# Optimization experiments

Measured on AMD Instinct MI355X. Metric: run time of the kernel, lower is better.

## Reference

```python
import jax, jax.numpy as jnp
import numpy as np

N = 128  # image size
J = 4    # number of scales
L = 4    # number of orientations


def make_morlet_filters(n, j_max, n_angles):
    """Fixed Morlet filter bank in Fourier space, shape [J, L, N, N] (real)."""
    freqs = np.fft.fftfreq(n) * 2.0 * np.pi
    kx = freqs[:, None] * np.ones((1, n))
    ky = np.ones((n, 1)) * freqs[None, :]
    filters = np.zeros((j_max, n_angles, n, n), dtype=np.float32)
    for j in range(j_max):
        k0 = 3.0 * np.pi / 4.0 / (2.0 ** j)   # central frequency of scale j
        sigma = 0.8 * (2.0 ** j)               # gaussian width in space
        for l in range(n_angles):
            theta = np.pi * l / n_angles
            k0x, k0y = k0 * np.cos(theta), k0 * np.sin(theta)
            beta = np.exp(-0.5 * sigma ** 2 * k0 ** 2)  # zero-mean correction
            g_shift = np.exp(-0.5 * sigma ** 2 * ((kx - k0x) ** 2 + (ky - k0y) ** 2))
            g_zero = np.exp(-0.5 * sigma ** 2 * (kx ** 2 + ky ** 2))
            filters[j, l] = g_shift - beta * g_zero
    return jnp.asarray(filters)


PSI = make_morlet_filters(N, J, L)  # fixed (non-learned) filter bank
VALID_PAIRS = [(j1, j2) for j1 in range(J) for j2 in range(J) if j2 > j1]  # 6 pairs


def setup_inputs() -> dict:
    key = jax.random.key(0)
    k1, k2, k3, k4, k5 = jax.random.split(key, 5)
    B = 64
    return {
        "image_batch": jax.random.normal(k1, (B, N, N), dtype=jnp.float32),
        "fc1_w": jax.random.normal(k2, (4, 11), dtype=jnp.float32) * 0.3,
        "fc1_b": jax.random.normal(k3, (4,), dtype=jnp.float32) * 0.1,
        "fc2_w": jax.random.normal(k4, (10, 4), dtype=jnp.float32) * 0.3,
        "fc2_b": jax.random.normal(k5, (10,), dtype=jnp.float32) * 0.1,
    }


def _scattering(image):
    # image: [B, N, N]
    i_hat = jnp.fft.fft2(image)  # [B,N,N] complex64
    s0 = jnp.mean(image, axis=(1, 2))  # [B]
    # first order: |x * psi_{j1,l1}|  -> [B,J,L,N,N]
    u1 = jnp.abs(jnp.fft.ifft2(i_hat[:, None, None] * PSI[None]))
    s1 = jnp.mean(u1, axis=(2, 3, 4))  # [B,J] averaged over orientations+space
    u1_hat = jnp.fft.fft2(u1)  # [B,J,L,N,N]
    # second order: only j2 > j1 (others NaN in original and masked out)
    s2_list = []
    for (j1, j2) in VALID_PAIRS:
        # [B, L1, L2, N, N]
        field = jnp.fft.ifft2(u1_hat[:, j1, :, None] * PSI[j2][None, None])
        s2_list.append(jnp.mean(jnp.abs(field), axis=(1, 2, 3, 4)))
    s2 = jnp.stack(s2_list, axis=1)  # [B,6]
    return jnp.concatenate([s0[:, None], s1, s2], axis=1)  # [B,11]


def reference(image_batch, fc1_w, fc1_b, fc2_w, fc2_b):
    coeffs = _scattering(image_batch)                      # [B,11]
    h = jax.nn.relu(coeffs @ fc1_w.T + fc1_b)              # [B,4]
    return jax.nn.sigmoid(h @ fc2_w.T + fc2_b)             # [B,10]
```

## Files before the change

### kernel.cpp

```cpp
#include <hip/hip_runtime.h>
#include <math.h>

#define NN   128
#define SS   129
#define TT   512
#define NPIX 16384
#define EPT  32
#define SG   65
#define SG32 33


__device__ __forceinline__ float2 cmul(float2 a, float2 w) {
    return make_float2(a.x * w.x - a.y * w.y, a.x * w.y + a.y * w.x);
}
__device__ __forceinline__ float2 cmulc(float2 a, float2 w) {
    return make_float2(a.x * w.x + a.y * w.y, a.y * w.x - a.x * w.y);
}

template<int SGN>
__device__ __forceinline__ void fft4(float2* f) {
    float2 t0 = make_float2(f[0].x + f[2].x, f[0].y + f[2].y);
    float2 t1 = make_float2(f[0].x - f[2].x, f[0].y - f[2].y);
    float2 t2 = make_float2(f[1].x + f[3].x, f[1].y + f[3].y);
    float2 t3 = make_float2(f[1].x - f[3].x, f[1].y - f[3].y);
// ... 380 lines not shown
        int fb = blk - 256;
        int f = fb >> 3, chunk = fb & 7;
        int j = f >> 2, l = f & 3;
        float k0    = 2.35619449019234493f / (float)(1 << j);
        float sigma = 0.8f * (float)(1 << j);
        float s2    = sigma * sigma;
        float theta = 0.78539816339744831f * (float)l;
        float k0x = k0 * cosf(theta);
        float k0y = k0 * sinf(theta);
        float beta = expf(-0.5f * s2 * k0 * k0);
        const float FSTEP = 0.04908738521234052f;
        float* dst = psi + (size_t)f * NPIX;
        int i0 = chunk * 2048, i1 = i0 + 2048;
        for (int i = i0 + tid; i < i1; i += TT) {
            int pr = i >> 7, pc = i & 127;
            int kr = (pr >> 4) + 8 * (pr & 15);
            int kc = (pc >> 4) + 8 * (pc & 15);
            float fr = (float)(kr < 64 ? kr : kr - 128) * FSTEP;
            float fc = (float)(kc < 64 ? kc : kc - 128) * FSTEP;
            float dx = fr - k0x, dy = fc - k0y;
            float g1 = expf(-0.5f * s2 * (dx * dx + dy * dy));
            float g0 = expf(-0.5f * s2 * (fr * fr + fc * fc));
            dst[i] = g1 - beta * g0;
        }
        return;
    }
    int b = blk >> 2, q = blk & 3;
    buildTw(tw, tid);
    const float* im = img + (size_t)b * NPIX + (size_t)q * 32 * NN;
    #pragma unroll
    for (int k = 0; k < 8; ++k) {
        int e = k * TT + tid;
        F[(e >> 7) * SS + (e & 127)] = make_float2(im[e], 0.f);
    }
    __syncthreads();
    {
        int x = tid & 31, t = tid >> 5;
        float2* M = F + x * SS;
        float2 f[8];
        #pragma unroll
        for (int n1 = 0; n1 < 8; ++n1) f[n1] = M[t + 16 * n1];
        fft8<-1>(f);
        #pragma unroll
        for (int ka = 0; ka < 8; ++ka)
            M[t + 16 * ka] = cmulc(f[ka], tw[t * ka]);
    }
    __syncthreads();
    if (tid < 256) {
        int x = tid & 31, ka = tid >> 5;
        float2* M = F + x * SS + 16 * ka;
        float2 g[16];
        #pragma unroll
        for (int t = 0; t < 16; ++t) g[t] = M[t];
        fft16<-1>(g);
        #pragma unroll
        for (int kb = 0; kb < 16; ++kb) M[kb] = g[kb];
    }
    __syncthreads();
    float2* dst = interm + (size_t)b * NPIX + (size_t)q * 32 * NN;
    #pragma unroll
    for (int k = 0; k < 8; ++k) {
        int e = k * TT + tid;
        dst[e] = F[(e >> 7) * SS + (e & 127)];
    }
}

__global__ __attribute__((amdgpu_flat_work_group_size(TT, TT), amdgpu_waves_per_eu(4, 4)))
void k_pre2(float2* __restrict__ ihat,
            float* __restrict__ coeffs) {
    __shared__ __align__(16) float2 F[128 * 33];
    __shared__ float2 tw[128];
    int blk = blockIdx.x, tid = threadIdx.x;
    int b = blk >> 2, q = blk & 3;
    buildTw(tw, tid);
    float2* base = ihat + (size_t)b * NPIX + q * 32;
    #pragma unroll
    for (int k = 0; k < 8; ++k) {
        int e = k * TT + tid;
        int r = e >> 5, cl = e & 31;
        F[r * 33 + cl] = base[r * NN + cl];
    }
    __syncthreads();
    {
        int cl = tid & 31, t = tid >> 5;
        float2 f[8];
        #pragma unroll
        for (int n1 = 0; n1 < 8; ++n1) f[n1] = F[(t + 16 * n1) * 33 + cl];
        fft8<-1>(f);
        #pragma unroll
        for (int ka = 0; ka < 8; ++ka)
            F[(t + 16 * ka) * 33 + cl] = cmulc(f[ka], tw[t * ka]);
    }
    __syncthreads();
    if (tid < 256) {
        int cl = tid & 31, ka = tid >> 5;
        float2 g[16];
        #pragma unroll
        for (int t = 0; t < 16; ++t) g[t] = F[(16 * ka + t) * 33 + cl];
        fft16<-1>(g);
        float2* dst = base + cl;
        #pragma unroll
        for (int kb = 0; kb < 16; ++kb)
            dst[(16 * ka + kb) * NN] = g[kb];
        if (q == 0 && cl == 0 && ka == 0)
            coeffs[b * 11 + 0] = g[0].x * (1.f / 16384.f);
    }
}

__global__ __attribute__((amdgpu_flat_work_group_size(TT, TT), amdgpu_waves_per_eu(2, 2)))
void k_scat_big(const float2* __restrict__ ihat,
                const float* __restrict__ psi,
                float* __restrict__ coeffs,
                float2* __restrict__ Hg) {
    __shared__ __align__(16) float2 F[16640];
    __shared__ float2 tw[128];
    float2* G2a = F;
    float2* G2b = F + 4160;
    float2* G2c = F + 8320;
    float2* G2d = F + 12480;
    int tid = threadIdx.x;
    int x = blockIdx.x;
    int b = x & 63, l1 = x >> 6;
    const float2* ih = ihat + (size_t)b * NPIX;
    const float*  p1 = psi + (size_t)l1 * NPIX;
    buildTw(tw, tid);

    const float S1_128 = 9.3132257461547852e-10f;
    const float S2TR   = 5.6843418860808015e-14f;

    int kalo = tid >> 7, c = tid & 127;
    {
        #pragma unroll
        for (int i = 0; i < 2; ++i) {
            int ka = kalo + 4 * i;
            float2 g[16];
            #pragma unroll
            for (int kb = 0; kb < 16; ++kb) {
                int e = (16 * ka + kb) * NN + c;
                float2 z = ih[e];
                float  p = p1[e];
                g[kb] = make_float2(z.x * p, z.y * p);
            }
            fft16<1>(g);
            #pragma unroll
            for (int t = 0; t < 16; ++t)
                F[(16 * ka + t) * SS + c] = cmul(g[t], tw[t * ka]);
        }
    }
    __syncthreads();
    invB<SS, 1>(F, tid);      __syncthreads();
    invA<1, SS>(F, tw, tid);  __syncthreads();
    float acc = 0.f;
    invBmag_fwdA_row(F, tw, tid, acc);
    float ws1 = waveReduceSum(acc);
    if ((tid & 63) == 0) atomicAdd(&coeffs[b * 11 + 1], ws1 * S1_128);
    __syncthreads();
    fwdB<1, SS>(F, tid);      __syncthreads();
    fwdA<SS, 1>(F, tw, tid);  __syncthreads();
    float2 uh[32];
    fwdB_col_capture(F, tid, uh);
    __syncthreads();

    int m = c & 15;
    bool colKeep = (m < 4) || (m >= 12);
    int pc64 = 8 * (c >> 4) + ((m < 4) ? m : (m - 8));
    int fc = (c >> 4) + 8 * (c & 15);

    {
        float2* Hf = Hg + ((size_t)(b * 4 + l1)) * 4096;
        if (colKeep) {
            #pragma unroll
            for (int i = 0; i < 2; ++i) {
                int ka = kalo + 4 * i;
                #pragma unroll
                for (int kb = 0; kb < 16; ++kb) {
                    if (kb < 4 || kb >= 12) {
                        int pr64 = 8 * ka + ((kb < 4) ? kb : (kb - 8));
                        Hf[pr64 * 64 + pc64] = uh[i * 16 + kb];
                    }
                }
            }
        }
    }

    {
        const int ORW[4] = {21, 15, 0, -15};
        const int OCW[4] = { 0, 15, 21,  15};
        bool ckw[4]; int pcw[4];
        #pragma unroll
        for (int w = 0; w < 4; ++w) {
            int dc = (fc - OCW[w]) & 127;
            ckw[w] = (dc < 32) || (dc >= 96);
            int uc = (dc < 32) ? dc : (dc - 64);
            pcw[w] = 8 * (uc & 7) + (uc >> 3);
        }
        #pragma unroll
        for (int i = 0; i < 2; ++i) {
            int ka = kalo + 4 * i;
            #pragma unroll
            for (int kb = 0; kb < 16; ++kb) {
                int fr = ka + 8 * kb;
                float2 z = uh[i * 16 + kb];
                int e = (16 * ka + kb) * NN + c;
                #pragma unroll
                for (int w = 0; w < 4; ++w) {
                    if (ckw[w]) {
                        int dr = (fr - ORW[w]) & 127;
                        if (dr < 32 || dr >= 96) {
                            int ur = (dr < 32) ? dr : (dr - 64);
                            int pr = 8 * (ur & 7) + (ur >> 3);
                            float pv = psi[(size_t)(4 + w) * NPIX + e];
                            float2* G = (w == 0) ? G2a : (w == 1) ? G2b
                                       : (w == 2) ? G2c : G2d;
                            G[pr * SG + pcw[w]] = make_float2(z.x * pv, z.y * pv);
                        }
                    }
                }
            }
        }
        __syncthreads();
        {
            int col = tid & 63, k8 = tid >> 6;
            float2 f0[8], f1[8], f2[8], f3[8];
            #pragma unroll
            for (int kb = 0; kb < 8; ++kb) {
                int o = (8 * k8 + kb) * SG + col;
                f0[kb] = G2a[o]; f1[kb] = G2b[o]; f2[kb] = G2c[o]; f3[kb] = G2d[o];
            }
            fft8<1>(f0); fft8<1>(f1); fft8<1>(f2); fft8<1>(f3);
            #pragma unroll
            for (int q = 0; q < 8; ++q) {
                float2 w = tw[2 * q * k8];
                int o = (8 * k8 + q) * SG + col;
                G2a[o] = cmul(f0[q], w); G2b[o] = cmul(f1[q], w);
                G2c[o] = cmul(f2[q], w); G2d[o] = cmul(f3[q], w);
            }
        }
        __syncthreads();
        {
            int col = tid & 63, q = tid >> 6;
            float2 f0[8], f1[8], f2[8], f3[8];
            #pragma unroll
            for (int k8 = 0; k8 < 8; ++k8) {
                int o = (8 * k8 + q) * SG + col;
                f0[k8] = G2a[o]; f1[k8] = G2b[o]; f2[k8] = G2c[o]; f3[k8] = G2d[o];
            }
            fft8<1>(f0); fft8<1>(f1); fft8<1>(f2); fft8<1>(f3);
            #pragma unroll
            for (int n1 = 0; n1 < 8; ++n1) {
                int o = (8 * n1 + q) * SG + col;
                G2a[o] = f0[n1]; G2b[o] = f1[n1]; G2c[o] = f2[n1]; G2d[o] = f3[n1];
            }
        }
        __syncthreads();
        {
            int row = tid & 63, k8 = tid >> 6;
            int base = row * SG + 8 * k8;
            float2 f0[8], f1[8], f2[8], f3[8];
            #pragma unroll
            for (int kb = 0; kb < 8; ++kb) {
                f0[kb] = G2a[base + kb]; f1[kb] = G2b[base + kb];
                f2[kb] = G2c[base + kb]; f3[kb] = G2d[base + kb];
            }
            fft8<1>(f0); fft8<1>(f1); fft8<1>(f2); fft8<1>(f3);
            #pragma unroll
            for (int q = 0; q < 8; ++q) {
                float2 w = tw[2 * q * k8];
                G2a[base + q] = cmul(f0[q], w); G2b[base + q] = cmul(f1[q], w);
                G2c[base + q] = cmul(f2[q], w); G2d[base + q] = cmul(f3[q], w);
            }
        }
        __syncthreads();
        float a2 = 0.f;
        {
            int row = tid & 63, q = tid >> 6;
            int base = row * SG + q;
            float2 f0[8], f1[8], f2[8], f3[8];
            #pragma unroll
            for (int k8 = 0; k8 < 8; ++k8) {
                int o = base + 8 * k8;
                f0[k8] = G2a[o]; f1[k8] = G2b[o]; f2[k8] = G2c[o]; f3[k8] = G2d[o];
            }
            fft8<1>(f0); fft8<1>(f1); fft8<1>(f2); fft8<1>(f3);
            #pragma unroll
            for (int n1 = 0; n1 < 8; ++n1) {
                a2 += sqrtf(f0[n1].x * f0[n1].x + f0[n1].y * f0[n1].y);
                a2 += sqrtf(f1[n1].x * f1[n1].x + f1[n1].y * f1[n1].y);
                a2 += sqrtf(f2[n1].x * f2[n1].x + f2[n1].y * f2[n1].y);
                a2 += sqrtf(f3[n1].x * f3[n1].x + f3[n1].y * f3[n1].y);
            }
        }
        float ws2 = waveReduceSum(a2);
        if ((tid & 63) == 0) atomicAdd(&coeffs[b * 11 + 5 + 0], ws2 * S2TR);
    }
}

__global__ __attribute__((amdgpu_flat_work_group_size(TT, TT), amdgpu_waves_per_eu(4, 4)))
void k_scat_small(const float2* __restrict__ ihat,
                  const float* __restrict__ psi,
                  float* __restrict__ coeffs,
                  const float2* __restrict__ Hg) {
    __shared__ __align__(16) float2 S[8448];
    __shared__ float2 tw[128];
    float2* G2  = S;
    float2* G32 = S;
    float2* Qs0 = S;
    float2* Qs1 = S + 1056;
    float2* Qs2 = S + 2112;
    float2* Qs3 = S + 3168;
    float4* Psa = (float4*)(S + 4224);
    float4* Psb = (float4*)(S + 6336);
    int tid = threadIdx.x;
    int x = blockIdx.x;
    int b = x & 63, l1 = (x >> 6) & 3;
    int t0 = x >> 8;
    const float2* ih = ihat + (size_t)b * NPIX;
    const float*  p1 = psi + (size_t)(((t0 == 0) ? 1 : ((t0 == 2) ? 2 : 3)) * 4 + l1) * NPIX;
    buildTw(tw, tid);

    const float S1_64 = 3.7252902984619141e-9f;
    const float S1_32 = 1.4901161193847656e-8f;
    const float S2_32 = 9.0949470177292824e-13f;

    int kalo = tid >> 7, c = tid & 127;

    if (t0 == 1) {
        const float S2_03 = 2.2737367544323206e-13f;
        const float2* Hf = Hg + ((size_t)(b * 4 + l1)) * 4096;
        int m = c & 15;
        bool colKeep = (m < 4) || (m >= 12);
        int pc64 = 8 * (c >> 4) + ((m < 4) ? m : (m - 8));
        int fc = (c >> 4) + 8 * (c & 15);
        const int OR2[4] = {9, 6, 0, -6};
        const int OC2[4] = {0, 6, 9,  6};
        bool ckq[4]; int pcq[4];
        #pragma unroll
        for (int w = 0; w < 4; ++w) {
            int dc = (fc - OC2[w]) & 127;
            ckq[w] = (dc < 16) || (dc >= 112);
            int f32c = (dc < 16) ? dc : (dc - 96);
            pcq[w] = 4 * (f32c & 7) + (f32c >> 3);
        }
        bool ck32 = (m < 2) || (m >= 14);
        int pc32 = 4 * (c >> 4) + ((m < 2) ? m : (m - 12));
        const float* p20 = psi + (size_t)8 * NPIX;
        const float* p30 = psi + (size_t)12 * NPIX;
        if (colKeep) {
            #pragma unroll
            for (int i = 0; i < 2; ++i) {
                int ka = kalo + 4 * i;
                #pragma unroll
                for (int kb = 0; kb < 16; ++kb) {
                    if (kb < 4 || kb >= 12) {
                        int pr64 = 8 * ka + ((kb < 4) ? kb : (kb - 8));
                        float2 z = Hf[pr64 * 64 + pc64];
                        int fr = ka + 8 * kb;
                        int e = (16 * ka + kb) * NN + c;
                        #pragma unroll
                        for (int w = 0; w < 4; ++w) {
                            if (ckq[w]) {
                                int dr = (fr - OR2[w]) & 127;
                                if (dr < 16 || dr >= 112) {
                                    int f32r = (dr < 16) ? dr : (dr - 96);
                                    int pr = 4 * (f32r & 7) + (f32r >> 3);
                                    float pv = p20[(size_t)w * NPIX + e];
                                    float2* Q = (w == 0) ? Qs0 : (w == 1) ? Qs1
                                               : (w == 2) ? Qs2 : Qs3;
                                    Q[pr * SG32 + pcq[w]] = make_float2(z.x * pv, z.y * pv);
                                }
                            }
                        }
                        if (ck32 && (kb < 2 || kb >= 14)) {
                            int pr32 = 4 * ka + ((kb < 2) ? kb : (kb - 12));
                            float a0 = p30[e], a1 = p30[NPIX + e];
                            float a2f = p30[2 * NPIX + e], a3 = p30[3 * NPIX + e];
                            Psa[pr32 * SG32 + pc32] =
                                make_float4(z.x * a0, z.y * a0, z.x * a1, z.y * a1);
                            Psb[pr32 * SG32 + pc32] =
                                make_float4(z.x * a2f, z.y * a2f, z.x * a3, z.y * a3);
                        }
                    }
                }
            }
        }
        float aq, ap;
        pass32combo(Qs0, Qs1, Qs2, Qs3, Psa, Psb, tw, tid, aq, ap);
        float wsq = waveReduceSum(aq);
        float wsp = waveReduceSum(ap);
        if ((tid & 63) == 0) {
            atomicAdd(&coeffs[b * 11 + 5 + 1], wsq * S2_03);
            atomicAdd(&coeffs[b * 11 + 5 + 2], wsp * S2_03);
        }
        return;
    }

    if (t0 == 0) {
        const int OR1[4] = {21, 15, 0, -15};
        const int OC1[4] = { 0, 15, 21,  15};
        int fc = (c >> 4) + 8 * (c & 15);
        int dc = (fc - OC1[l1]) & 127;
        bool ck = (dc < 32) || (dc >= 96);
        int ucw = (dc < 32) ? dc : (dc - 64);
        int pcd = 8 * (ucw & 7) + (ucw >> 3);
        if (ck) {
            #pragma unroll
            for (int i = 0; i < 2; ++i) {
                int ka = kalo + 4 * i;
                #pragma unroll
                for (int kb = 0; kb < 16; ++kb) {
                    int fr = ka + 8 * kb;
                    int dr = (fr - OR1[l1]) & 127;
                    if (dr < 32 || dr >= 96) {
                        int ur = (dr < 32) ? dr : (dr - 64);
                        int pr = 8 * (ur & 7) + (ur >> 3);
                        int e = (16 * ka + kb) * NN + c;
                        float2 z = ih[e];
                        float  p = p1[e];
                        G2[pr * SG + pcd] = make_float2(z.x * p, z.y * p);
                    }
                }
            }
        }
        __syncthreads();
        {
            int col = tid & 63, k8 = tid >> 6;
            float2 f[8];
            #pragma unroll
            for (int kb = 0; kb < 8; ++kb) f[kb] = G2[(8 * k8 + kb) * SG + col];
            fft8<1>(f);
            #pragma unroll
            for (int q = 0; q < 8; ++q)
                G2[(8 * k8 + q) * SG + col] = cmul(f[q], tw[2 * q * k8]);
        }
        __syncthreads();
        {
            int col = tid & 63, q = tid >> 6;
            float2 f[8];
            #pragma unroll
            for (int k8 = 0; k8 < 8; ++k8) f[k8] = G2[(8 * k8 + q) * SG + col];
            fft8<1>(f);
            #pragma unroll
            for (int n1 = 0; n1 < 8; ++n1) G2[(8 * n1 + q) * SG + col] = f[n1];
        }
        __syncthreads();
        {
            int row = tid & 63, k8 = tid >> 6;
            float2* R = G2 + row * SG + 8 * k8;
            float2 f[8];
            #pragma unroll
            for (int kb = 0; kb < 8; ++kb) f[kb] = R[kb];
            fft8<1>(f);
            #pragma unroll
            for (int q = 0; q < 8; ++q) R[q] = cmul(f[q], tw[2 * q * k8]);
        }
        __syncthreads();
        float acc = 0.f;
        {
            int row = tid & 63, q = tid >> 6;
            float2* R = G2 + row * SG + q;
            float2 f[8];
            #pragma unroll
            for (int k8 = 0; k8 < 8; ++k8) f[k8] = R[8 * k8];
            fft8<1>(f);
            #pragma unroll
            for (int n1 = 0; n1 < 8; ++n1) {
                float mg = sqrtf(f[n1].x * f[n1].x + f[n1].y * f[n1].y);
                acc += mg;
                f[n1] = make_float2(mg, 0.f);
            }
            fft8<-1>(f);
            #pragma unroll
            for (int ka = 0; ka < 8; ++ka)
                R[8 * ka] = cmulc(f[ka], tw[2 * q * ka]);
        }
        float ws1 = waveReduceSum(acc);
        if ((tid & 63) == 0) atomicAdd(&coeffs[b * 11 + 2], ws1 * S1_64);
        __syncthreads();
        {
            int row2 = tid & 63, ka = tid >> 6;
            float2* R2 = G2 + row2 * SG + 8 * ka;
            float2 g[8];
            #pragma unroll
            for (int t = 0; t < 8; ++t) g[t] = R2[t];
            fft8<-1>(g);
            #pragma unroll
            for (int kb = 0; kb < 8; ++kb) R2[kb] = g[kb];
        }
        __syncthreads();
        {
            int col = tid & 63, t = tid >> 6;
            float2 g[8];
            #pragma unroll
            for (int n1 = 0; n1 < 8; ++n1) g[n1] = G2[(t + 8 * n1) * SG + col];
            fft8<-1>(g);
            #pragma unroll
            for (int ka = 0; ka < 8; ++ka)
                G2[(t + 8 * ka) * SG + col] = cmulc(g[ka], tw[2 * t * ka]);
        }
        __syncthreads();
        float2 vh[8];
        int c6 = tid & 63, ka8 = tid >> 6;
        {
            float2 g[8];
            #pragma unroll
            for (int t = 0; t < 8; ++t) g[t] = G2[(8 * ka8 + t) * SG + c6];
            fft8<-1>(g);
            #pragma unroll
            for (int kb = 0; kb < 8; ++kb) vh[kb] = g[kb];
        }
        __syncthreads();

        int uc64 = 8 * (c6 & 7) + (c6 >> 3);
        int fc128 = (uc64 < 32) ? uc64 : (uc64 + 64);
        int scI = 16 * (fc128 & 7) + (fc128 >> 3);
        int se[8];
        #pragma unroll
        for (int kb = 0; kb < 8; ++kb) {
            int ur = 8 * kb + ka8;
            int fr128 = (ur < 32) ? ur : (ur + 64);
            se[kb] = (16 * (fr128 & 7) + (fr128 >> 3)) * NN + scI;
        }

        {
            const int OR2[4] = {9, 6, 0, -6};
            const int OC2[4] = {0, 6, 9,  6};
            bool ckq[4]; int pcq[4];
            #pragma unroll
            for (int w = 0; w < 4; ++w) {
                int dcw = (uc64 - OC2[w]) & 63;
                ckq[w] = (dcw < 16) || (dcw >= 48);
                int f32c = (dcw < 16) ? dcw : (dcw - 32);
                pcq[w] = 4 * (f32c & 7) + (f32c >> 3);
            }
            int m6 = c6 & 7;
            bool ckV = (m6 < 2) || (m6 >= 6);
            int p32c = 4 * (c6 >> 3) + ((m6 < 2) ? m6 : (m6 - 4));
            const float* p30 = psi + (size_t)12 * NPIX;
            #pragma unroll
            for (int kb = 0; kb < 8; ++kb) {
                int ur = 8 * kb + ka8;
                float2 z = vh[kb];
                int e = se[kb];
                #pragma unroll
                for (int w = 0; w < 4; ++w) {
                    if (ckq[w]) {
                        int dr = (ur - OR2[w]) & 63;
                        if (dr < 16 || dr >= 48) {
                            int f32r = (dr < 16) ? dr : (dr - 32);
                            int pr = 4 * (f32r & 7) + (f32r >> 3);
                            float pv = psi[(size_t)(8 + w) * NPIX + e];
                            float2* Q = (w == 0) ? Qs0 : (w == 1) ? Qs1
                                       : (w == 2) ? Qs2 : Qs3;
                            Q[pr * SG32 + pcq[w]] = make_float2(z.x * pv, z.y * pv);
                        }
                    }
                }
                if (ckV && (kb < 2 || kb >= 6)) {
                    int pr32 = 4 * ka8 + (kb & 3);
                    float a0 = p30[e], a1 = p30[NPIX + e];
                    float a2f = p30[2 * NPIX + e], a3 = p30[3 * NPIX + e];
                    Psa[pr32 * SG32 + p32c] =
                        make_float4(z.x * a0, z.y * a0, z.x * a1, z.y * a1);
                    Psb[pr32 * SG32 + p32c] =
                        make_float4(z.x * a2f, z.y * a2f, z.x * a3, z.y * a3);
                }
            }
            float aq, ap;
            pass32combo(Qs0, Qs1, Qs2, Qs3, Psa, Psb, tw, tid, aq, ap);
            float wsq = waveReduceSum(aq);
            float wsp = waveReduceSum(ap);
            if ((tid & 63) == 0) {
                atomicAdd(&coeffs[b * 11 + 5 + 3], wsq * S2_32);
                atomicAdd(&coeffs[b * 11 + 5 + 4], wsp * S2_32);
            }
        }
        return;
    }

    if (t0 == 3) {
        int m = c & 15;
        bool ck32 = (m < 2) || (m >= 14);
        int pc32 = 4 * (c >> 4) + ((m < 2) ? m : (m - 12));
        if (ck32) {
            #pragma unroll
            for (int i = 0; i < 2; ++i) {
                int ka = kalo + 4 * i;
                #pragma unroll
                for (int kb = 0; kb < 16; ++kb) {
                    if (kb < 2 || kb >= 14) {
                        int e = (16 * ka + kb) * NN + c;
                        float2 z = ih[e];
                        float  p = p1[e];
                        int pr32 = 4 * ka + ((kb < 2) ? kb : (kb - 12));
                        G32[pr32 * SG32 + pc32] = make_float2(z.x * p, z.y * p);
                    }
                }
            }
        }
        __syncthreads();
        if (tid < 256) {
            int line = tid & 31, a = tid >> 5;
            float2 f[4];
            #pragma unroll
            for (int kb = 0; kb < 4; ++kb) f[kb] = G32[(4 * a + kb) * SG32 + line];
            fft4<1>(f);
            #pragma unroll
            for (int t = 0; t < 4; ++t)
                G32[(4 * a + t) * SG32 + line] = cmul(f[t], tw[4 * t * a]);
        }
        __syncthreads();
        if (tid < 128) {
            int line = tid & 31, t = tid >> 5;
            float2 f[8];
            #pragma unroll
            for (int a = 0; a < 8; ++a) f[a] = G32[(4 * a + t) * SG32 + line];
            fft8<1>(f);
            #pragma unroll
            for (int n1 = 0; n1 < 8; ++n1) G32[(4 * n1 + t) * SG32 + line] = f[n1];
        }
        __syncthreads();
        if (tid < 256) {
            int row = tid & 31, a = tid >> 5;
            float2* R = G32 + row * SG32 + 4 * a;
            float2 f[4];
            #pragma unroll
            for (int kb = 0; kb < 4; ++kb) f[kb] = R[kb];
            fft4<1>(f);
            #pragma unroll
            for (int t = 0; t < 4; ++t) R[t] = cmul(f[t], tw[4 * t * a]);
        }
        __syncthreads();
        float acc = 0.f;
        if (tid < 128) {
            int row = tid & 31, t = tid >> 5;
            float2* R = G32 + row * SG32 + t;
            float2 f[8];
            #pragma unroll
            for (int a = 0; a < 8; ++a) f[a] = R[4 * a];
            fft8<1>(f);
            #pragma unroll
            for (int n1 = 0; n1 < 8; ++n1)
                acc += sqrtf(f[n1].x * f[n1].x + f[n1].y * f[n1].y);
        }
        float ws1 = waveReduceSum(acc);
        if ((tid & 63) == 0 && tid < 128) atomicAdd(&coeffs[b * 11 + 4], ws1 * S1_32);
        return;
    }

    {
        const float S2_23 = 3.6379788070917130e-12f;
        const int OR1[4] = {9, 6, 0, -6};
        const int OC1[4] = {0, 6, 9,  6};
        float2* G = S;
        float4* Pa = (float4*)(S + 1088);
        float4* Pb = (float4*)(S + 3200);
        int fc = (c >> 4) + 8 * (c & 15);
        int dc = (fc - OC1[l1]) & 127;
        bool ck = (dc < 16) || (dc >= 112);
        int f32c = (dc < 16) ? dc : (dc - 96);
        int pcd = 4 * (f32c & 7) + (f32c >> 3);
        if (ck) {
            #pragma unroll
            for (int i = 0; i < 2; ++i) {
                int ka = kalo + 4 * i;
                #pragma unroll
                for (int kb = 0; kb < 16; ++kb) {
                    int fr = ka + 8 * kb;
                    int dr = (fr - OR1[l1]) & 127;
                    if (dr < 16 || dr >= 112) {
                        int f32r = (dr < 16) ? dr : (dr - 96);
                        int pr = 4 * (f32r & 7) + (f32r >> 3);
                        int e = (16 * ka + kb) * NN + c;
                        float2 z = ih[e];
                        float  p = p1[e];
                        G[pr * SG32 + pcd] = make_float2(z.x * p, z.y * p);
                    }
                }
            }
        }
        __syncthreads();
        if (tid < 256) {
            int line = tid & 31, a = tid >> 5;
            float2 f[4];
            #pragma unroll
            for (int kb = 0; kb < 4; ++kb) f[kb] = G[(4 * a + kb) * SG32 + line];
            fft4<1>(f);
            #pragma unroll
            for (int t = 0; t < 4; ++t)
                G[(4 * a + t) * SG32 + line] = cmul(f[t], tw[4 * t * a]);
        }
        __syncthreads();
        if (tid < 128) {
            int line = tid & 31, t = tid >> 5;
            float2 f[8];
            #pragma unroll
            for (int a = 0; a < 8; ++a) f[a] = G[(4 * a + t) * SG32 + line];
            fft8<1>(f);
            #pragma unroll
            for (int n1 = 0; n1 < 8; ++n1) G[(4 * n1 + t) * SG32 + line] = f[n1];
        }
        __syncthreads();
        if (tid < 256) {
            int row = tid & 31, a = tid >> 5;
            float2* R = G + row * SG32 + 4 * a;
            float2 f[4];
            #pragma unroll
            for (int kb = 0; kb < 4; ++kb) f[kb] = R[kb];
            fft4<1>(f);
            #pragma unroll
            for (int t = 0; t < 4; ++t) R[t] = cmul(f[t], tw[4 * t * a]);
        }
        __syncthreads();
        float acc = 0.f;
        if (tid < 128) {
            int row = tid & 31, t = tid >> 5;
            float2* R = G + row * SG32 + t;
            float2 f[8];
            #pragma unroll
            for (int a = 0; a < 8; ++a) f[a] = R[4 * a];
            fft8<1>(f);
            #pragma unroll
            for (int n1 = 0; n1 < 8; ++n1) {
                float mg = sqrtf(f[n1].x * f[n1].x + f[n1].y * f[n1].y);
                acc += mg;
                R[4 * n1] = make_float2(mg, 0.f);
            }
        }
        float ws1 = waveReduceSum(acc);
        if ((tid & 63) == 0 && tid < 128) atomicAdd(&coeffs[b * 11 + 3], ws1 * S1_32);
        __syncthreads();
        if (tid < 256) {
            int row = tid & 31, a = tid >> 5;
            float2* R = G + row * SG32 + 4 * a;
            float2 f[4];
            #pragma unroll
            for (int kb = 0; kb < 4; ++kb) f[kb] = R[kb];
            fft4<-1>(f);
            #pragma unroll
            for (int t = 0; t < 4; ++t) R[t] = cmulc(f[t], tw[4 * t * a]);
        }
        __syncthreads();
        if (tid < 128) {
            int row = tid & 31, t = tid >> 5;
            float2* R = G + row * SG32 + t;
            float2 f[8];
            #pragma unroll
            for (int a = 0; a < 8; ++a) f[a] = R[4 * a];
            fft8<-1>(f);
            #pragma unroll
            for (int n1 = 0; n1 < 8; ++n1) R[4 * n1] = f[n1];
        }
        __syncthreads();
        if (tid < 256) {
            int line = tid & 31, a = tid >> 5;
            float2 f[4];
            #pragma unroll
            for (int kb = 0; kb < 4; ++kb) f[kb] = G[(4 * a + kb) * SG32 + line];
            fft4<-1>(f);
            #pragma unroll
            for (int t = 0; t < 4; ++t)
                G[(4 * a + t) * SG32 + line] = cmulc(f[t], tw[4 * t * a]);
        }
        __syncthreads();
        if (tid < 128) {
            int line = tid & 31, t = tid >> 5;
            float2 f[8];
            #pragma unroll
            for (int a = 0; a < 8; ++a) f[a] = G[(4 * a + t) * SG32 + line];
            fft8<-1>(f);
            #pragma unroll
            for (int n1 = 0; n1 < 8; ++n1) G[(4 * n1 + t) * SG32 + line] = f[n1];
        }
        __syncthreads();
        {
            const float* q0 = psi + (size_t)12 * NPIX;
            const float* q1 = q0 + NPIX;
            const float* q2 = q1 + NPIX;
            const float* q3 = q2 + NPIX;
            #pragma unroll
            for (int ii = 0; ii < 2; ++ii) {
                int s = ii * 512 + tid;
                int pr = s >> 5, pc = s & 31;
                int ur = (pr >> 2) + 8 * (pr & 3);
                int uc = (pc >> 2) + 8 * (pc & 3);
                int fr = (ur < 16) ? ur : (ur + 96);
                int fcc = (uc < 16) ? uc : (uc + 96);
                int e = (16 * (fr & 7) + (fr >> 3)) * NN
                      + 16 * (fcc & 7) + (fcc >> 3);
                float2 z = G[pr * SG32 + pc];
                float a0 = q0[e], a1 = q1[e], a2f = q2[e], a3 = q3[e];
                Pa[pr * SG32 + pc] = make_float4(z.x * a0, z.y * a0, z.x * a1, z.y * a1);
                Pb[pr * SG32 + pc] = make_float4(z.x * a2f, z.y * a2f, z.x * a3, z.y * a3);
            }
        }
        float a2 = pass32x4(Pa, Pb, tw, tid);
        float ws2 = waveReduceSum(a2);
        if ((tid & 63) == 0) atomicAdd(&coeffs[b * 11 + 5 + 5], ws2 * S2_23);
    }
}

__global__ void k_mlp(const float* __restrict__ coeffs,
                      const float* __restrict__ w1, const float* __restrict__ b1,
                      const float* __restrict__ w2, const float* __restrict__ b2,
                      float* __restrict__ out) {
    int b = threadIdx.x;
    if (b >= 64) return;
    float c[11];
    #pragma unroll
    for (int i = 0; i < 11; ++i) c[i] = coeffs[b * 11 + i];
    float h[4];
    #pragma unroll
    for (int k = 0; k < 4; ++k) {
        float s = b1[k];
        #pragma unroll
        for (int i = 0; i < 11; ++i) s += w1[k * 11 + i] * c[i];
        h[k] = fmaxf(s, 0.f);
    }
    #pragma unroll
    for (int o = 0; o < 10; ++o) {
        float s = b2[o];
        #pragma unroll
        for (int k = 0; k < 4; ++k) s += w2[o * 4 + k] * h[k];
        out[b * 10 + o] = 1.f / (1.f + expf(-s));
    }
}

extern "C" void kernel_launch(void* const* d_in, const int* in_sizes, int n_in,
                              void* d_out, int out_size, void* d_ws, size_t ws_size,
                              hipStream_t stream) {
    const float* img = (const float*)d_in[0];
    const float* w1  = (const float*)d_in[1];
    const float* b1  = (const float*)d_in[2];
    const float* w2  = (const float*)d_in[3];
    const float* b2  = (const float*)d_in[4];
    float* out = (float*)d_out;

    float*  ws     = (float*)d_ws;
    float*  psi    = ws;
    float2* ihat   = (float2*)(ws + 16 * NPIX);
    float2* Hg     = ihat + (size_t)64 * NPIX;
    float*  coeffs = ws + 16 * NPIX + 2 * 64 * NPIX + 2 * 256 * 4096;

    hipLaunchKernelGGL(k_pre1,       dim3(385),  dim3(TT), 0, stream, img, psi, ihat, coeffs);
    hipLaunchKernelGGL(k_pre2,       dim3(256),  dim3(TT), 0, stream, ihat, coeffs);
    hipLaunchKernelGGL(k_scat_big,   dim3(256),  dim3(TT), 0, stream, ihat, psi, coeffs, Hg);
    hipLaunchKernelGGL(k_scat_small, dim3(1024), dim3(TT), 0, stream, ihat, psi, coeffs, Hg);
    hipLaunchKernelGGL(k_mlp,        dim3(1),    dim3(64), 0, stream, coeffs, w1, b1, w2, b2, out);
}
```

Baseline: 167.9 us.

## Pair j1=1 orientations per block and schedule heavy blocks first

The j1=1 scattering branch now has each block process two orientations. The two orientations share the image-spectrum loads, and the block runs both 64x64 FFT pipelines in lockstep between the same barriers. The second-order stage then loops over the two fields, reusing the shared-memory scratch. Block indices are remapped so these heavier blocks come first in the grid, which shrinks from 1024 to 896 blocks. The aim is to cut redundant global loads and reduce tail imbalance, at the cost of longer per-block critical paths and higher register pressure.

```diff
diff --git a/kernel.cpp b/kernel.cpp
--- a/kernel.cpp
+++ b/kernel.cpp
@@ -706,7 +706,6 @@
                   const float2* __restrict__ Hg) {
     __shared__ __align__(16) float2 S[8448];
     __shared__ float2 tw[128];
-    float2* G2  = S;
     float2* G32 = S;
     float2* Qs0 = S;
     float2* Qs1 = S + 1056;
@@ -716,10 +715,6 @@
     float4* Psb = (float4*)(S + 6336);
     int tid = threadIdx.x;
     int x = blockIdx.x;
-    int b = x & 63, l1 = (x >> 6) & 3;
-    int t0 = x >> 8;
-    const float2* ih = ihat + (size_t)b * NPIX;
-    const float*  p1 = psi + (size_t)(((t0 == 0) ? 1 : ((t0 == 2) ? 2 : 3)) * 4 + l1) * NPIX;
     buildTw(tw, tid);
 
     const float S1_64 = 3.7252902984619141e-9f;
@@ -728,7 +723,298 @@
 
     int kalo = tid >> 7, c = tid & 127;
 
-    if (t0 == 1) {
+    if (x < 128) {
+        int b = x & 63, ph = x >> 6;
+        int l1a = 2 * ph, l1b = 2 * ph + 1;
+        const float2* ih = ihat + (size_t)b * NPIX;
+        const float* p1a = psi + (size_t)(4 + l1a) * NPIX;
+        const float* p1b = psi + (size_t)(4 + l1b) * NPIX;
+        float2* G2A = S;
+        float2* G2B = S + 4160;
+        const int OR1[4] = {21, 15, 0, -15};
+        const int OC1[4] = { 0, 15, 21,  15};
+        int fc = (c >> 4) + 8 * (c & 15);
+        int dcA = (fc - OC1[l1a]) & 127;
+        bool ckA = (dcA < 32) || (dcA >= 96);
+        int ucwA = (dcA < 32) ? dcA : (dcA - 64);
+        int pcdA = 8 * (ucwA & 7) + (ucwA >> 3);
+        int dcB = (fc - OC1[l1b]) & 127;
+        bool ckB = (dcB < 32) || (dcB >= 96);
+        int ucwB = (dcB < 32) ? dcB : (dcB - 64);
+        int pcdB = 8 * (ucwB & 7) + (ucwB >> 3);
+        #pragma unroll
+        for (int i = 0; i < 2; ++i) {
+            int ka = kalo + 4 * i;
+            #pragma unroll
+            for (int kb = 0; kb < 16; ++kb) {
+                int fr = ka + 8 * kb;
+                int e = (16 * ka + kb) * NN + c;
+                float2 z = ih[e];
+                if (ckA) {
+                    int dr = (fr - OR1[l1a]) & 127;
+                    if (dr < 32 || dr >= 96) {
+                        int ur = (dr < 32) ? dr : (dr - 64);
+                        int pr = 8 * (ur & 7) + (ur >> 3);
+                        float p = p1a[e];
+                        G2A[pr * SG + pcdA] = make_float2(z.x * p, z.y * p);
+                    }
+                }
+                if (ckB) {
+                    int dr = (fr - OR1[l1b]) & 127;
+                    if (dr < 32 || dr >= 96) {
+                        int ur = (dr < 32) ? dr : (dr - 64);
+                        int pr = 8 * (ur & 7) + (ur >> 3);
+                        float p = p1b[e];
+                        G2B[pr * SG + pcdB] = make_float2(z.x * p, z.y * p);
+                    }
+                }
+            }
+        }
+        __syncthreads();
+        {
+            int col = tid & 63, k8 = tid >> 6;
+            {
+                float2 f[8];
+                #pragma unroll
+                for (int kb = 0; kb < 8; ++kb) f[kb] = G2A[(8 * k8 + kb) * SG + col];
+                fft8<1>(f);
+                #pragma unroll
+                for (int q = 0; q < 8; ++q)
+                    G2A[(8 * k8 + q) * SG + col] = cmul(f[q], tw[2 * q * k8]);
+            }
+            {
+                float2 f[8];
+                #pragma unroll
+                for (int kb = 0; kb < 8; ++kb) f[kb] = G2B[(8 * k8 + kb) * SG + col];
+                fft8<1>(f);
+                #pragma unroll
+                for (int q = 0; q < 8; ++q)
+                    G2B[(8 * k8 + q) * SG + col] = cmul(f[q], tw[2 * q * k8]);
+            }
+        }
+        __syncthreads();
+        {
+            int col = tid & 63, q = tid >> 6;
+            {
+                float2 f[8];
+                #pragma unroll
+                for (int k8 = 0; k8 < 8; ++k8) f[k8] = G2A[(8 * k8 + q) * SG + col];
+                fft8<1>(f);
+                #pragma unroll
+                for (int n1 = 0; n1 < 8; ++n1) G2A[(8 * n1 + q) * SG + col] = f[n1];
+            }
+            {
+                float2 f[8];
+                #pragma unroll
+                for (int k8 = 0; k8 < 8; ++k8) f[k8] = G2B[(8 * k8 + q) * SG + col];
+                fft8<1>(f);
+                #pragma unroll
+                for (int n1 = 0; n1 < 8; ++n1) G2B[(8 * n1 + q) * SG + col] = f[n1];
+            }
+        }
+        __syncthreads();
+        {
+            int row = tid & 63, k8 = tid >> 6;
+            {
+                float2* R = G2A + row * SG + 8 * k8;
+                float2 f[8];
+                #pragma unroll
+                for (int kb = 0; kb < 8; ++kb) f[kb] = R[kb];
+                fft8<1>(f);
+                #pragma unroll
+                for (int q = 0; q < 8; ++q) R[q] = cmul(f[q], tw[2 * q * k8]);
+            }
+            {
+                float2* R = G2B + row * SG + 8 * k8;
+                float2 f[8];
+                #pragma unroll
+                for (int kb = 0; kb < 8; ++kb) f[kb] = R[kb];
+                fft8<1>(f);
+                #pragma unroll
+                for (int q = 0; q < 8; ++q) R[q] = cmul(f[q], tw[2 * q * k8]);
+            }
+        }
+        __syncthreads();
+        float acc = 0.f;
+        {
+            int row = tid & 63, q = tid >> 6;
+            {
+                float2* R = G2A + row * SG + q;
+                float2 f[8];
+                #pragma unroll
+                for (int k8 = 0; k8 < 8; ++k8) f[k8] = R[8 * k8];
+                fft8<1>(f);
+                #pragma unroll
+                for (int n1 = 0; n1 < 8; ++n1) {
+                    float mg = sqrtf(f[n1].x * f[n1].x + f[n1].y * f[n1].y);
+                    acc += mg;
+                    f[n1] = make_float2(mg, 0.f);
+                }
+                fft8<-1>(f);
+                #pragma unroll
+                for (int ka = 0; ka < 8; ++ka)
+                    R[8 * ka] = cmulc(f[ka], tw[2 * q * ka]);
+            }
+            {
+                float2* R = G2B + row * SG + q;
+                float2 f[8];
+                #pragma unroll
+                for (int k8 = 0; k8 < 8; ++k8) f[k8] = R[8 * k8];
+                fft8<1>(f);
+                #pragma unroll
+                for (int n1 = 0; n1 < 8; ++n1) {
+                    float mg = sqrtf(f[n1].x * f[n1].x + f[n1].y * f[n1].y);
+                    acc += mg;
+                    f[n1] = make_float2(mg, 0.f);
+                }
+                fft8<-1>(f);
+                #pragma unroll
+                for (int ka = 0; ka < 8; ++ka)
+                    R[8 * ka] = cmulc(f[ka], tw[2 * q * ka]);
+            }
+        }
+        float ws1 = waveReduceSum(acc);
+        if ((tid & 63) == 0) atomicAdd(&coeffs[b * 11 + 2], ws1 * S1_64);
+        __syncthreads();
+        {
+            int row2 = tid & 63, ka = tid >> 6;
+            {
+                float2* R2 = G2A + row2 * SG + 8 * ka;
+                float2 g[8];
+                #pragma unroll
+                for (int t = 0; t < 8; ++t) g[t] = R2[t];
+                fft8<-1>(g);
+                #pragma unroll
+                for (int kb = 0; kb < 8; ++kb) R2[kb] = g[kb];
+            }
+            {
+                float2* R2 = G2B + row2 * SG + 8 * ka;
+                float2 g[8];
+                #pragma unroll
+                for (int t = 0; t < 8; ++t) g[t] = R2[t];
+                fft8<-1>(g);
+                #pragma unroll
+                for (int kb = 0; kb < 8; ++kb) R2[kb] = g[kb];
+            }
+        }
+        __syncthreads();
+        {
+            int col = tid & 63, t = tid >> 6;
+            {
+                float2 g[8];
+                #pragma unroll
+                for (int n1 = 0; n1 < 8; ++n1) g[n1] = G2A[(t + 8 * n1) * SG + col];
+                fft8<-1>(g);
+                #pragma unroll
+                for (int ka = 0; ka < 8; ++ka)
+                    G2A[(t + 8 * ka) * SG + col] = cmulc(g[ka], tw[2 * t * ka]);
+            }
+            {
+                float2 g[8];
+                #pragma unroll
+                for (int n1 = 0; n1 < 8; ++n1) g[n1] = G2B[(t + 8 * n1) * SG + col];
+                fft8<-1>(g);
+                #pragma unroll
+                for (int ka = 0; ka < 8; ++ka)
+                    G2B[(t + 8 * ka) * SG + col] = cmulc(g[ka], tw[2 * t * ka]);
+            }
+        }
+        __syncthreads();
+        float2 vhA[8], vhB[8];
+        int c6 = tid & 63, ka8 = tid >> 6;
+        {
+            {
+                float2 g[8];
+                #pragma unroll
+                for (int t = 0; t < 8; ++t) g[t] = G2A[(8 * ka8 + t) * SG + c6];
+                fft8<-1>(g);
+                #pragma unroll
+                for (int kb = 0; kb < 8; ++kb) vhA[kb] = g[kb];
+            }
+            {
+                float2 g[8];
+                #pragma unroll
+                for (int t = 0; t < 8; ++t) g[t] = G2B[(8 * ka8 + t) * SG + c6];
+                fft8<-1>(g);
+                #pragma unroll
+                for (int kb = 0; kb < 8; ++kb) vhB[kb] = g[kb];
+            }
+        }
+        __syncthreads();
+
+        int uc64 = 8 * (c6 & 7) + (c6 >> 3);
+        int fc128 = (uc64 < 32) ? uc64 : (uc64 + 64);
+        int scI = 16 * (fc128 & 7) + (fc128 >> 3);
+        int se[8];
+        #pragma unroll
+        for (int kb = 0; kb < 8; ++kb) {
+            int ur = 8 * kb + ka8;
+            int fr128 = (ur < 32) ? ur : (ur + 64);
+            se[kb] = (16 * (fr128 & 7) + (fr128 >> 3)) * NN + scI;
+        }
+        const int OR2[4] = {9, 6, 0, -6};
+        const int OC2[4] = {0, 6, 9,  6};
+        bool ckq[4]; int pcq[4];
+        #pragma unroll
+        for (int w = 0; w < 4; ++w) {
+            int dcw = (uc64 - OC2[w]) & 63;
+            ckq[w] = (dcw < 16) || (dcw >= 48);
+            int f32c = (dcw < 16) ? dcw : (dcw - 32);
+            pcq[w] = 4 * (f32c & 7) + (f32c >> 3);
+        }
+        int m6 = c6 & 7;
+        bool ckV = (m6 < 2) || (m6 >= 6);
+        int p32c = 4 * (c6 >> 3) + ((m6 < 2) ? m6 : (m6 - 4));
+        const float* p30 = psi + (size_t)12 * NPIX;
+
+        #pragma unroll
+        for (int fld = 0; fld < 2; ++fld) {
+            const float2* vh = (fld == 0) ? vhA : vhB;
+            #pragma unroll
+            for (int kb = 0; kb < 8; ++kb) {
+                int ur = 8 * kb + ka8;
+                float2 z = vh[kb];
+                int e = se[kb];
+                #pragma unroll
+                for (int w = 0; w < 4; ++w) {
+                    if (ckq[w]) {
+                        int dr = (ur - OR2[w]) & 63;
+                        if (dr < 16 || dr >= 48) {
+                            int f32r = (dr < 16) ? dr : (dr - 32);
+                            int pr = 4 * (f32r & 7) + (f32r >> 3);
+                            float pv = psi[(size_t)(8 + w) * NPIX + e];
+                            float2* Q = (w == 0) ? Qs0 : (w == 1) ? Qs1
+                                       : (w == 2) ? Qs2 : Qs3;
+                            Q[pr * SG32 + pcq[w]] = make_float2(z.x * pv, z.y * pv);
+                        }
+                    }
+                }
+                if (ckV && (kb < 2 || kb >= 6)) {
+                    int pr32 = 4 * ka8 + (kb & 3);
+                    float a0 = p30[e], a1 = p30[NPIX + e];
+                    float a2f = p30[2 * NPIX + e], a3 = p30[3 * NPIX + e];
+                    Psa[pr32 * SG32 + p32c] =
+                        make_float4(z.x * a0, z.y * a0, z.x * a1, z.y * a1);
+                    Psb[pr32 * SG32 + p32c] =
+                        make_float4(z.x * a2f, z.y * a2f, z.x * a3, z.y * a3);
+                }
+            }
+            float aq, ap;
+            pass32combo(Qs0, Qs1, Qs2, Qs3, Psa, Psb, tw, tid, aq, ap);
+            float wsq = waveReduceSum(aq);
+            float wsp = waveReduceSum(ap);
+            if ((tid & 63) == 0) {
+                atomicAdd(&coeffs[b * 11 + 5 + 3], wsq * S2_32);
+                atomicAdd(&coeffs[b * 11 + 5 + 4], wsp * S2_32);
+            }
+            __syncthreads();
+        }
+        return;
+    }
+
+    if (x < 384) {
+        int y = x - 128;
+        int b = y & 63, l1 = y >> 6;
         const float S2_03 = 2.2737367544323206e-13f;
         const float2* Hf = Hg + ((size_t)(b * 4 + l1)) * 4096;
         int m = c & 15;
@@ -798,260 +1084,11 @@
         return;
     }
 
-    if (t0 == 0) {
-        const int OR1[4] = {21, 15, 0, -15};
-        const int OC1[4] = { 0, 15, 21,  15};
-        int fc = (c >> 4) + 8 * (c & 15);
-        int dc = (fc - OC1[l1]) & 127;
-        bool ck = (dc < 32) || (dc >= 96);
-        int ucw = (dc < 32) ? dc : (dc - 64);
-        int pcd = 8 * (ucw & 7) + (ucw >> 3);
-        if (ck) {
-            #pragma unroll
-            for (int i = 0; i < 2; ++i) {
-                int ka = kalo + 4 * i;
-                #pragma unroll
-                for (int kb = 0; kb < 16; ++kb) {
-                    int fr = ka + 8 * kb;
-                    int dr = (fr - OR1[l1]) & 127;
-                    if (dr < 32 || dr >= 96) {
-                        int ur = (dr < 32) ? dr : (dr - 64);
-                        int pr = 8 * (ur & 7) + (ur >> 3);
-                        int e = (16 * ka + kb) * NN + c;
-                        float2 z = ih[e];
-                        float  p = p1[e];
-                        G2[pr * SG + pcd] = make_float2(z.x * p, z.y * p);
-                    }
-                }
-            }
-        }
-        __syncthreads();
-        {
-            int col = tid & 63, k8 = tid >> 6;
-            float2 f[8];
-            #pragma unroll
-            for (int kb = 0; kb < 8; ++kb) f[kb] = G2[(8 * k8 + kb) * SG + col];
-            fft8<1>(f);
-            #pragma unroll
-            for (int q = 0; q < 8; ++q)
-                G2[(8 * k8 + q) * SG + col] = cmul(f[q], tw[2 * q * k8]);
-        }
-        __syncthreads();
-        {
-            int col = tid & 63, q = tid >> 6;
-            float2 f[8];
-            #pragma unroll
-            for (int k8 = 0; k8 < 8; ++k8) f[k8] = G2[(8 * k8 + q) * SG + col];
-            fft8<1>(f);
-            #pragma unroll
-            for (int n1 = 0; n1 < 8; ++n1) G2[(8 * n1 + q) * SG + col] = f[n1];
-        }
-        __syncthreads();
-        {
-            int row = tid & 63, k8 = tid >> 6;
-            float2* R = G2 + row * SG + 8 * k8;
-            float2 f[8];
-            #pragma unroll
-            for (int kb = 0; kb < 8; ++kb) f[kb] = R[kb];
-            fft8<1>(f);
-            #pragma unroll
-            for (int q = 0; q < 8; ++q) R[q] = cmul(f[q], tw[2 * q * k8]);
-        }
-        __syncthreads();
-        float acc = 0.f;
-        {
-            int row = tid & 63, q = tid >> 6;
-            float2* R = G2 + row * SG + q;
-            float2 f[8];
-            #pragma unroll
-            for (int k8 = 0; k8 < 8; ++k8) f[k8] = R[8 * k8];
-            fft8<1>(f);
-            #pragma unroll
-            for (int n1 = 0; n1 < 8; ++n1) {
-                float mg = sqrtf(f[n1].x * f[n1].x + f[n1].y * f[n1].y);
-                acc += mg;
-                f[n1] = make_float2(mg, 0.f);
-            }
-            fft8<-1>(f);
-            #pragma unroll
-            for (int ka = 0; ka < 8; ++ka)
-                R[8 * ka] = cmulc(f[ka], tw[2 * q * ka]);
-        }
-        float ws1 = waveReduceSum(acc);
-        if ((tid & 63) == 0) atomicAdd(&coeffs[b * 11 + 2], ws1 * S1_64);
-        __syncthreads();
-        {
-            int row2 = tid & 63, ka = tid >> 6;
-            float2* R2 = G2 + row2 * SG + 8 * ka;
-            float2 g[8];
-            #pragma unroll
-            for (int t = 0; t < 8; ++t) g[t] = R2[t];
-            fft8<-1>(g);
-            #pragma unroll
-            for (int kb = 0; kb < 8; ++kb) R2[kb] = g[kb];
-        }
-        __syncthreads();
-        {
-            int col = tid & 63, t = tid >> 6;
-            float2 g[8];
-            #pragma unroll
-            for (int n1 = 0; n1 < 8; ++n1) g[n1] = G2[(t + 8 * n1) * SG + col];
-            fft8<-1>(g);
-            #pragma unroll
-            for (int ka = 0; ka < 8; ++ka)
-                G2[(t + 8 * ka) * SG + col] = cmulc(g[ka], tw[2 * t * ka]);
-        }
-        __syncthreads();
-        float2 vh[8];
-        int c6 = tid & 63, ka8 = tid >> 6;
-        {
-            float2 g[8];
-            #pragma unroll
-            for (int t = 0; t < 8; ++t) g[t] = G2[(8 * ka8 + t) * SG + c6];
-            fft8<-1>(g);
-            #pragma unroll
-            for (int kb = 0; kb < 8; ++kb) vh[kb] = g[kb];
-        }
-        __syncthreads();
-
-        int uc64 = 8 * (c6 & 7) + (c6 >> 3);
-        int fc128 = (uc64 < 32) ? uc64 : (uc64 + 64);
-        int scI = 16 * (fc128 & 7) + (fc128 >> 3);
-        int se[8];
-        #pragma unroll
-        for (int kb = 0; kb < 8; ++kb) {
-            int ur = 8 * kb + ka8;
-            int fr128 = (ur < 32) ? ur : (ur + 64);
-            se[kb] = (16 * (fr128 & 7) + (fr128 >> 3)) * NN + scI;
-        }
-
-        {
-            const int OR2[4] = {9, 6, 0, -6};
-            const int OC2[4] = {0, 6, 9,  6};
-            bool ckq[4]; int pcq[4];
-            #pragma unroll
-            for (int w = 0; w < 4; ++w) {
-                int dcw = (uc64 - OC2[w]) & 63;
-                ckq[w] = (dcw < 16) || (dcw >= 48);
-                int f32c = (dcw < 16) ? dcw : (dcw - 32);
-                pcq[w] = 4 * (f32c & 7) + (f32c >> 3);
-            }
-            int m6 = c6 & 7;
-            bool ckV = (m6 < 2) || (m6 >= 6);
-            int p32c = 4 * (c6 >> 3) + ((m6 < 2) ? m6 : (m6 - 4));
-            const float* p30 = psi + (size_t)12 * NPIX;
-            #pragma unroll
-            for (int kb = 0; kb < 8; ++kb) {
-                int ur = 8 * kb + ka8;
-                float2 z = vh[kb];
-                int e = se[kb];
-                #pragma unroll
-                for (int w = 0; w < 4; ++w) {
-                    if (ckq[w]) {
-                        int dr = (ur - OR2[w]) & 63;
-                        if (dr < 16 || dr >= 48) {
-                            int f32r = (dr < 16) ? dr : (dr - 32);
-                            int pr = 4 * (f32r & 7) + (f32r >> 3);
-                            float pv = psi[(size_t)(8 + w) * NPIX + e];
-                            float2* Q = (w == 0) ? Qs0 : (w == 1) ? Qs1
-                                       : (w == 2) ? Qs2 : Qs3;
-                            Q[pr * SG32 + pcq[w]] = make_float2(z.x * pv, z.y * pv);
-                        }
-                    }
-                }
-                if (ckV && (kb < 2 || kb >= 6)) {
-                    int pr32 = 4 * ka8 + (kb & 3);
-                    float a0 = p30[e], a1 = p30[NPIX + e];
-                    float a2f = p30[2 * NPIX + e], a3 = p30[3 * NPIX + e];
-                    Psa[pr32 * SG32 + p32c] =
-                        make_float4(z.x * a0, z.y * a0, z.x * a1, z.y * a1);
-                    Psb[pr32 * SG32 + p32c] =
-                        make_float4(z.x * a2f, z.y * a2f, z.x * a3, z.y * a3);
-                }
-            }
-            float aq, ap;
-            pass32combo(Qs0, Qs1, Qs2, Qs3, Psa, Psb, tw, tid, aq, ap);
-            float wsq = waveReduceSum(aq);
-            float wsp = waveReduceSum(ap);
-            if ((tid & 63) == 0) {
-                atomicAdd(&coeffs[b * 11 + 5 + 3], wsq * S2_32);
-                atomicAdd(&coeffs[b * 11 + 5 + 4], wsp * S2_32);
-            }
-        }
-        return;
-    }
-
-    if (t0 == 3) {
-        int m = c & 15;
-        bool ck32 = (m < 2) || (m >= 14);
-        int pc32 = 4 * (c >> 4) + ((m < 2) ? m : (m - 12));
-        if (ck32) {
-            #pragma unroll
-            for (int i = 0; i < 2; ++i) {
-                int ka = kalo + 4 * i;
-                #pragma unroll
-                for (int kb = 0; kb < 16; ++kb) {
-                    if (kb < 2 || kb >= 14) {
-                        int e = (16 * ka + kb) * NN + c;
-                        float2 z = ih[e];
-                        float  p = p1[e];
-                        int pr32 = 4 * ka + ((kb < 2) ? kb : (kb - 12));
-                        G32[pr32 * SG32 + pc32] = make_float2(z.x * p, z.y * p);
-                    }
-                }
-            }
-        }
-        __syncthreads();
-        if (tid < 256) {
-            int line = tid & 31, a = tid >> 5;
-            float2 f[4];
-            #pragma unroll
-            for (int kb = 0; kb < 4; ++kb) f[kb] = G32[(4 * a + kb) * SG32 + line];
-            fft4<1>(f);
-            #pragma unroll
-            for (int t = 0; t < 4; ++t)
-                G32[(4 * a + t) * SG32 + line] = cmul(f[t], tw[4 * t * a]);
-        }
-        __syncthreads();
-        if (tid < 128) {
-            int line = tid & 31, t = tid >> 5;
-            float2 f[8];
-            #pragma unroll
-            for (int a = 0; a < 8; ++a) f[a] = G32[(4 * a + t) * SG32 + line];
-            fft8<1>(f);
-            #pragma unroll
-            for (int n1 = 0; n1 < 8; ++n1) G32[(4 * n1 + t) * SG32 + line] = f[n1];
-        }
-        __syncthreads();
-        if (tid < 256) {
-            int row = tid & 31, a = tid >> 5;
-            float2* R = G32 + row * SG32 + 4 * a;
-            float2 f[4];
-            #pragma unroll
-            for (int kb = 0; kb < 4; ++kb) f[kb] = R[kb];
-            fft4<1>(f);
-            #pragma unroll
-            for (int t = 0; t < 4; ++t) R[t] = cmul(f[t], tw[4 * t * a]);
-        }
-        __syncthreads();
-        float acc = 0.f;
-        if (tid < 128) {
-            int row = tid & 31, t = tid >> 5;
-            float2* R = G32 + row * SG32 + t;
-            float2 f[8];
-            #pragma unroll
-            for (int a = 0; a < 8; ++a) f[a] = R[4 * a];
-            fft8<1>(f);
-            #pragma unroll
-            for (int n1 = 0; n1 < 8; ++n1)
-                acc += sqrtf(f[n1].x * f[n1].x + f[n1].y * f[n1].y);
-        }
-        float ws1 = waveReduceSum(acc);
-        if ((tid & 63) == 0 && tid < 128) atomicAdd(&coeffs[b * 11 + 4], ws1 * S1_32);
-        return;
-    }
-
-    {
+    if (x < 640) {
+        int y = x - 384;
+        int b = y & 63, l1 = y >> 6;
+        const float2* ih = ihat + (size_t)b * NPIX;
+        const float* p1 = psi + (size_t)(8 + l1) * NPIX;
         const float S2_23 = 3.6379788070917130e-12f;
         const int OR1[4] = {9, 6, 0, -6};
         const int OC1[4] = {0, 6, 9,  6};
@@ -1200,6 +1237,80 @@
         float a2 = pass32x4(Pa, Pb, tw, tid);
         float ws2 = waveReduceSum(a2);
         if ((tid & 63) == 0) atomicAdd(&coeffs[b * 11 + 5 + 5], ws2 * S2_23);
+        return;
+    }
+
+    {
+        int y = x - 640;
+        int b = y & 63, l1 = y >> 6;
+        const float2* ih = ihat + (size_t)b * NPIX;
+        const float* p1 = psi + (size_t)(12 + l1) * NPIX;
+        int m = c & 15;
+        bool ck32 = (m < 2) || (m >= 14);
+        int pc32 = 4 * (c >> 4) + ((m < 2) ? m : (m - 12));
+        if (ck32) {
+            #pragma unroll
+            for (int i = 0; i < 2; ++i) {
+                int ka = kalo + 4 * i;
+                #pragma unroll
+                for (int kb = 0; kb < 16; ++kb) {
+                    if (kb < 2 || kb >= 14) {
+                        int e = (16 * ka + kb) * NN + c;
+                        float2 z = ih[e];
+                        float  p = p1[e];
+                        int pr32 = 4 * ka + ((kb < 2) ? kb : (kb - 12));
+                        G32[pr32 * SG32 + pc32] = make_float2(z.x * p, z.y * p);
+                    }
+                }
+            }
+        }
+        __syncthreads();
+        if (tid < 256) {
+            int line = tid & 31, a = tid >> 5;
+            float2 f[4];
+            #pragma unroll
+            for (int kb = 0; kb < 4; ++kb) f[kb] = G32[(4 * a + kb) * SG32 + line];
+            fft4<1>(f);
+            #pragma unroll
+            for (int t = 0; t < 4; ++t)
+                G32[(4 * a + t) * SG32 + line] = cmul(f[t], tw[4 * t * a]);
+        }
+        __syncthreads();
+        if (tid < 128) {
+            int line = tid & 31, t = tid >> 5;
+            float2 f[8];
+            #pragma unroll
+            for (int a = 0; a < 8; ++a) f[a] = G32[(4 * a + t) * SG32 + line];
+            fft8<1>(f);
+            #pragma unroll
+            for (int n1 = 0; n1 < 8; ++n1) G32[(4 * n1 + t) * SG32 + line] = f[n1];
+        }
+        __syncthreads();
+        if (tid < 256) {
+            int row = tid & 31, a = tid >> 5;
+            float2* R = G32 + row * SG32 + 4 * a;
+            float2 f[4];
+            #pragma unroll
+            for (int kb = 0; kb < 4; ++kb) f[kb] = R[kb];
+            fft4<1>(f);
+            #pragma unroll
+            for (int t = 0; t < 4; ++t) R[t] = cmul(f[t], tw[4 * t * a]);
+        }
+        __syncthreads();
+        float acc = 0.f;
+        if (tid < 128) {
+            int row = tid & 31, t = tid >> 5;
+            float2* R = G32 + row * SG32 + t;
+            float2 f[8];
+            #pragma unroll
+            for (int a = 0; a < 8; ++a) f[a] = R[4 * a];
+            fft8<1>(f);
+            #pragma unroll
+            for (int n1 = 0; n1 < 8; ++n1)
+                acc += sqrtf(f[n1].x * f[n1].x + f[n1].y * f[n1].y);
+        }
+        float ws1 = waveReduceSum(acc);
+        if ((tid & 63) == 0 && tid < 128) atomicAdd(&coeffs[b * 11 + 4], ws1 * S1_32);
     }
 }
 
@@ -1245,9 +1356,9 @@
     float2* Hg     = ihat + (size_t)64 * NPIX;
     float*  coeffs = ws + 16 * NPIX + 2 * 64 * NPIX + 2 * 256 * 4096;
 
-    hipLaunchKernelGGL(k_pre1,       dim3(385),  dim3(TT), 0, stream, img, psi, ihat, coeffs);
-    hipLaunchKernelGGL(k_pre2,       dim3(256),  dim3(TT), 0, stream, ihat, coeffs);
-    hipLaunchKernelGGL(k_scat_big,   dim3(256),  dim3(TT), 0, stream, ihat, psi, coeffs, Hg);
-    hipLaunchKernelGGL(k_scat_small, dim3(1024), dim3(TT), 0, stream, ihat, psi, coeffs, Hg);
-    hipLaunchKernelGGL(k_mlp,        dim3(1),    dim3(64), 0, stream, coeffs, w1, b1, w2, b2, out);
-}
+    hipLaunchKernelGGL(k_pre1,       dim3(385), dim3(TT), 0, stream, img, psi, ihat, coeffs);
+    hipLaunchKernelGGL(k_pre2,       dim3(256), dim3(TT), 0, stream, ihat, coeffs);
+    hipLaunchKernelGGL(k_scat_big,   dim3(256), dim3(TT), 0, stream, ihat, psi, coeffs, Hg);
+    hipLaunchKernelGGL(k_scat_small, dim3(896), dim3(TT), 0, stream, ihat, psi, coeffs, Hg);
+    hipLaunchKernelGGL(k_mlp,        dim3(1),   dim3(64), 0, stream, coeffs, w1, b1, w2, b2, out);
+}
```

Result: slower. 186.5 us (+11.0%).
